# Kernel tuning notes

Hardware: AMD Instinct MI355X
Metric: run time of the kernel (lower is better)

The kernel has to match this reference:

```python
import jax, jax.numpy as jnp
import numpy as np

POS_IOU, NEG_IOU = 0.5, 0.4
VAR = (0.1, 0.1, 0.2, 0.2)
ALPHA = 1.0
B, A, C, G = 16, 65536, 81, 32


def setup_inputs() -> dict:
    key = jax.random.key(0)
    k1, k2, k3, k4, k5, k6, k7 = jax.random.split(key, 7)
    cls_logits = jax.random.normal(k1, (B, A, C), dtype=jnp.float32)
    bbox_regs = jax.random.normal(k2, (B, A, 4), dtype=jnp.float32)
    # anchors: normalized cx,cy in (0,1), w,h positive
    anc_cxy = jax.random.uniform(k3, (A, 2), minval=0.05, maxval=0.95)
    anc_wh = jax.random.uniform(k4, (A, 2), minval=0.02, maxval=0.30)
    anchors_cxcywh = jnp.concatenate([anc_cxy, anc_wh], axis=-1).astype(jnp.float32)
    # GT boxes: valid normalized xyxy built from random cxcywh
    g_cxy = jax.random.uniform(k5, (B, G, 2), minval=0.1, maxval=0.9)
    g_wh = jax.random.uniform(k6, (B, G, 2), minval=0.05, maxval=0.40)
    x1y1 = jnp.clip(g_cxy - g_wh / 2, 0.0, 1.0)
    x2y2 = jnp.clip(g_cxy + g_wh / 2, 0.0, 1.0)
    gt_boxes = jnp.concatenate([x1y1, x2y2], axis=-1).astype(jnp.float32)
    gt_labels = jax.random.randint(k7, (B, G), 1, C).astype(jnp.int64)
    gt_valid = jnp.ones((B, G), dtype=bool)
    return {"cls_logits": cls_logits, "bbox_regs": bbox_regs,
            "anchors_cxcywh": anchors_cxcywh, "gt_boxes": gt_boxes,
            "gt_labels": gt_labels, "gt_valid": gt_valid}


def _encode(gt_xyxy, anc_cxcywh):
    # gt_xyxy [B,A,4], anc_cxcywh [A,4] -> offsets [B,A,4]
    x1, y1, x2, y2 = jnp.split(gt_xyxy, 4, axis=-1)
    gx, gy = (x1 + x2) / 2, (y1 + y2) / 2
    gw = jnp.clip(x2 - x1, 1e-6, None)
    gh = jnp.clip(y2 - y1, 1e-6, None)
    ax, ay, aw, ah = (anc_cxcywh[None, :, i:i + 1] for i in range(4))
    dx = (gx - ax) / (aw * VAR[0])
    dy = (gy - ay) / (ah * VAR[1])
    dw = jnp.log(gw / aw) / VAR[2]
    dh = jnp.log(gh / ah) / VAR[3]
    return jnp.concatenate([dx, dy, dw, dh], axis=-1)


def _forward(cls_logits, bbox_regs, anchors_cxcywh, gt_boxes, gt_labels, gt_valid):
    ax, ay, aw, ah = (anchors_cxcywh[:, i] for i in range(4))
    anc_xyxy = jnp.stack([ax - aw / 2, ay - ah / 2, ax + aw / 2, ay + ah / 2], axis=-1)  # [A,4]
    # IoU [B,A,G] (assignment is torch.no_grad in the original)
    tl = jnp.maximum(anc_xyxy[None, :, None, :2], gt_boxes[:, None, :, :2])
    br = jnp.minimum(anc_xyxy[None, :, None, 2:], gt_boxes[:, None, :, 2:])
    wh = jnp.clip(br - tl, 0.0, None)
    inter = wh[..., 0] * wh[..., 1]
    area_a = jnp.clip(anc_xyxy[:, 2] - anc_xyxy[:, 0], 0.0, None) * jnp.clip(anc_xyxy[:, 3] - anc_xyxy[:, 1], 0.0, None)
    area_b = jnp.clip(gt_boxes[..., 2] - gt_boxes[..., 0], 0.0, None) * jnp.clip(gt_boxes[..., 3] - gt_boxes[..., 1], 0.0, None)
    iou = inter / (area_a[None, :, None] + area_b[:, None, :] - inter + 1e-9)
    iou = jnp.where(gt_valid[:, None, :], iou, -1.0)  # padded GTs never match
    iou = jax.lax.stop_gradient(iou)

    iou_max = jnp.max(iou, axis=-1)              # [B,A]
    iou_idx = jnp.argmax(iou, axis=-1)           # [B,A]
    pos = iou_max >= POS_IOU
    ign = (iou_max > NEG_IOU) & ~pos

    matched_boxes = jnp.take_along_axis(gt_boxes, iou_idx[..., None], axis=1)   # [B,A,4]
    matched_labels = jnp.take_along_axis(gt_labels, iou_idx, axis=1)            # [B,A]
    cls_t = jnp.where(pos, matched_labels, jnp.where(ign, -1, 0))               # [B,A]
    reg_t = jax.lax.stop_gradient(_encode(matched_boxes, anchors_cxcywh))       # [B,A,4]

    # classification CE over valid (non-ignored) anchors, per-image mean
    logp = jax.nn.log_softmax(cls_logits, axis=-1)
    tgt = jnp.clip(cls_t, 0, None)
    ce = -jnp.take_along_axis(logp, tgt[..., None], axis=-1)[..., 0]            # [B,A]
    valid = cls_t >= 0
    n_valid = jnp.sum(valid, axis=1)
    cls_per = jnp.sum(ce * valid, axis=1) / jnp.maximum(n_valid, 1)
    total_cls = jnp.sum(jnp.where(n_valid > 0, cls_per, 0.0))

    # smooth L1 over positive anchors, per-image mean over pos*4 elements
    d = jnp.abs(bbox_regs - reg_t)
    sl1 = jnp.where(d < 1.0, 0.5 * d * d, d - 0.5)                              # [B,A,4]
    n_pos = jnp.sum(pos, axis=1)
    reg_per = jnp.sum(sl1 * pos[..., None], axis=(1, 2)) / jnp.maximum(4 * n_pos, 1)
    total_reg = jnp.sum(jnp.where(n_pos > 0, reg_per, 0.0))

    return total_cls + ALPHA * total_reg


def reference(cls_logits, bbox_regs, anchors_cxcywh, gt_boxes, gt_labels, gt_valid):
    return _forward(cls_logits, bbox_regs, anchors_cxcywh, gt_boxes, gt_labels, gt_valid)
```

## Files before the change

kernel.cpp:

```cpp
#include <hip/hip_runtime.h>
#include <math.h>

constexpr int kB = 16;
constexpr int kA = 65536;
constexpr int kC = 81;
constexpr int kG = 32;
constexpr int kBlockA = 256;
constexpr float kPosIou = 0.5f;
constexpr float kNegIou = 0.4f;

__global__ __launch_bounds__(256) void ssd_main_kernel(
    const float* __restrict__ cls_logits,
    const float* __restrict__ bbox_regs,
    const float* __restrict__ anchors,
    const float* __restrict__ gt_boxes,
    const int*   __restrict__ gt_labels,
    const int*   __restrict__ gt_valid,
    float* __restrict__ ws)
{
    __shared__ float s_gx1[kG], s_gy1[kG], s_gx2[kG], s_gy2[kG], s_area[kG];
    __shared__ int   s_lab[kG], s_val[kG];
    __shared__ int   s_t[kBlockA];
    __shared__ float s_red[4][4];

    const int tid = threadIdx.x;
    const int blocks_per_b = kA / kBlockA;
    const int b  = blockIdx.x / blocks_per_b;
    const int a0 = (blockIdx.x % blocks_per_b) * kBlockA;

    if (tid < kG) {
        float4 gb = *reinterpret_cast<const float4*>(gt_boxes + ((size_t)b * kG + tid) * 4);
        s_gx1[tid] = gb.x; s_gy1[tid] = gb.y; s_gx2[tid] = gb.z; s_gy2[tid] = gb.w;
        s_area[tid] = fmaxf(gb.z - gb.x, 0.f) * fmaxf(gb.w - gb.y, 0.f);
        s_lab[tid] = gt_labels[b * kG + tid];
        s_val[tid] = gt_valid[b * kG + tid];
    }
    __syncthreads();

    const int a = a0 + tid;
    float4 anc = *reinterpret_cast<const float4*>(anchors + (size_t)a * 4);
    const float ax1 = anc.x - anc.z * 0.5f, ay1 = anc.y - anc.w * 0.5f;
    const float ax2 = anc.x + anc.z * 0.5f, ay2 = anc.y + anc.w * 0.5f;
    const float area_a = fmaxf(ax2 - ax1, 0.f) * fmaxf(ay2 - ay1, 0.f);

    float best = -2.0f;
    int   bidx = 0;
    #pragma unroll 8
    for (int g = 0; g < kG; ++g) {
        float tlx = fmaxf(ax1, s_gx1[g]);
        float tly = fmaxf(ay1, s_gy1[g]);
        float brx = fminf(ax2, s_gx2[g]);
        float bry = fminf(ay2, s_gy2[g]);
        float w = fmaxf(brx - tlx, 0.f);
        float h = fmaxf(bry - tly, 0.f);
        float inter = w * h;
        float iou = inter / (area_a + s_area[g] - inter + 1e-9f);
        iou = s_val[g] ? iou : -1.0f;
        if (iou > best) { best = iou; bidx = g; }
    }
    const bool pos = best >= kPosIou;
    const bool ign = (best > kNegIou) && !pos;
    const int cls_t = pos ? s_lab[bidx] : (ign ? -1 : 0);
    s_t[tid] = cls_t;

    float reg_sum = 0.f;
    if (pos) {
        float gx1 = s_gx1[bidx], gy1 = s_gy1[bidx], gx2 = s_gx2[bidx], gy2 = s_gy2[bidx];
        float gx = (gx1 + gx2) * 0.5f, gy = (gy1 + gy2) * 0.5f;
        float gw = fmaxf(gx2 - gx1, 1e-6f), gh = fmaxf(gy2 - gy1, 1e-6f);
        float dx = (gx - anc.x) / (anc.z * 0.1f);
        float dy = (gy - anc.y) / (anc.w * 0.1f);
        float dw = __logf(gw / anc.z) / 0.2f;
        float dh = __logf(gh / anc.w) / 0.2f;
        float4 br = *reinterpret_cast<const float4*>(bbox_regs + ((size_t)b * kA + a) * 4);
        float d0 = fabsf(br.x - dx), d1 = fabsf(br.y - dy);
        float d2 = fabsf(br.z - dw), d3 = fabsf(br.w - dh);
        reg_sum = (d0 < 1.f ? 0.5f * d0 * d0 : d0 - 0.5f)
                + (d1 < 1.f ? 0.5f * d1 * d1 : d1 - 0.5f)
                + (d2 < 1.f ? 0.5f * d2 * d2 : d2 - 0.5f)
                + (d3 < 1.f ? 0.5f * d3 * d3 : d3 - 0.5f);
    }
    __syncthreads();

    const int wave = tid >> 6;
    const int lane = tid & 63;
    const int g4   = lane >> 2;
    const int q    = lane & 3;
    float ce_acc = 0.f;

    #pragma unroll 2
    for (int it = 0; it < kBlockA / 64; ++it) {
        const int idx = it * 64 + wave * 16 + g4;
        const int ct  = s_t[idx];
        const float* row = cls_logits + ((size_t)b * kA + a0 + idx) * kC;

        float s = 0.f;
        #pragma unroll
        for (int k = 0; k < 5; ++k) {
            float4 v;
            __builtin_memcpy(&v, row + (k << 4) + (q << 2), 16);
            s += __expf(v.x) + __expf(v.y) + __expf(v.z) + __expf(v.w);
        }
        float tv = 0.f;
        if (q == 0) {
            s += __expf(row[80]);
            tv = row[ct < 0 ? 0 : ct];
        }
        s += __shfl_xor(s, 1);
        s += __shfl_xor(s, 2);
        if (q == 0 && ct >= 0)
            ce_acc += __logf(s) - tv;
    }

    float v0 = ce_acc;
    float v1 = (cls_t >= 0) ? 1.f : 0.f;
    float v2 = reg_sum;
    float v3 = pos ? 1.f : 0.f;
    #pragma unroll
    for (int off = 32; off > 0; off >>= 1) {
        v0 += __shfl_xor(v0, off);
        v1 += __shfl_xor(v1, off);
        v2 += __shfl_xor(v2, off);
        v3 += __shfl_xor(v3, off);
    }
    if (lane == 0) {
        s_red[wave][0] = v0; s_red[wave][1] = v1;
        s_red[wave][2] = v2; s_red[wave][3] = v3;
    }
    __syncthreads();
    if (tid < 4) {
        float acc = s_red[0][tid] + s_red[1][tid] + s_red[2][tid] + s_red[3][tid];
        atomicAdd(&ws[b * 4 + tid], acc);
    }
}

__global__ void ssd_final_kernel(const float* __restrict__ ws, float* __restrict__ out)
{
    const int lane = threadIdx.x;
    float v = 0.f;
    if (lane < kB) {
        float sce  = ws[lane * 4 + 0];
        float nval = ws[lane * 4 + 1];
        float ssl  = ws[lane * 4 + 2];
        float npos = ws[lane * 4 + 3];
        float cls = (nval > 0.f) ? sce / fmaxf(nval, 1.f) : 0.f;
        float reg = (npos > 0.f) ? ssl / fmaxf(4.f * npos, 1.f) : 0.f;
        v = cls + reg;
    }
    #pragma unroll
    for (int off = 1; off < kB; off <<= 1)
        v += __shfl_xor(v, off);
    if (lane == 0) out[0] = v;
}

extern "C" void kernel_launch(void* const* d_in, const int* in_sizes, int n_in,
                              void* d_out, int out_size, void* d_ws, size_t ws_size,
                              hipStream_t stream) {
    const float* cls_logits = (const float*)d_in[0];
    const float* bbox_regs  = (const float*)d_in[1];
    const float* anchors    = (const float*)d_in[2];
    const float* gt_boxes   = (const float*)d_in[3];
    const int*   gt_labels  = (const int*)d_in[4];
    const int*   gt_valid   = (const int*)d_in[5];
    float* ws  = (float*)d_ws;
    float* out = (float*)d_out;

    hipMemsetAsync(d_ws, 0, kB * 4 * sizeof(float), stream);

    ssd_main_kernel<<<dim3(kB * (kA / kBlockA)), dim3(kBlockA), 0, stream>>>(
        cls_logits, bbox_regs, anchors, gt_boxes, gt_labels, gt_valid, ws);
    ssd_final_kernel<<<dim3(1), dim3(64), 0, stream>>>(ws, out);
}
```

Before: 84.69 us.

## Stream logits with block-contiguous float4 loads and LDS atomic row sums

Each block now reads its contiguous 256x81 logits tile with fully coalesced float4 loads indexed linearly, computes exp per element and adds the results into per-row shared-memory sums. It uses LDS atomics spread over four banks in place of per-row 4-lane groups with misaligned loads. The per-batch global atomics and memset are replaced by per-block partial writes, which the final kernel reduces. The tradeoff is more LDS atomic traffic and an integer divide per float4 in exchange for better global memory coalescing.

New measurement: 144.5 us. +70.6%, slower.

```diff
diff --git a/kernel.cpp b/kernel.cpp
--- a/kernel.cpp
+++ b/kernel.cpp
@@ -6,8 +6,28 @@
 constexpr int kC = 81;
 constexpr int kG = 32;
 constexpr int kBlockA = 256;
+constexpr int kBlocksPerB = kA / kBlockA;
+constexpr int kSumStride = 264;
 constexpr float kPosIou = 0.5f;
 constexpr float kNegIou = 0.4f;
+
+__device__ __forceinline__ void accum_f4(float (*s_sum)[kSumStride], int bank,
+                                         const float* __restrict__ base, int j) {
+    float4 v = *reinterpret_cast<const float4*>(base + 4 * j);
+    const int f0 = 4 * j;
+    const int r = f0 / 81;
+    const int rem = f0 - r * 81;
+    const float e0 = __expf(v.x), e1 = __expf(v.y);
+    const float e2 = __expf(v.z), e3 = __expf(v.w);
+    if (rem <= 77) {
+        atomicAdd(&s_sum[bank][r], e0 + e1 + e2 + e3);
+    } else {
+        atomicAdd(&s_sum[bank][(f0 + 0) / 81], e0);
+        atomicAdd(&s_sum[bank][(f0 + 1) / 81], e1);
+        atomicAdd(&s_sum[bank][(f0 + 2) / 81], e2);
+        atomicAdd(&s_sum[bank][(f0 + 3) / 81], e3);
+    }
+}
 
 __global__ __launch_bounds__(256) void ssd_main_kernel(
     const float* __restrict__ cls_logits,
@@ -20,13 +40,12 @@
 {
     __shared__ float s_gx1[kG], s_gy1[kG], s_gx2[kG], s_gy2[kG], s_area[kG];
     __shared__ int   s_lab[kG], s_val[kG];
-    __shared__ int   s_t[kBlockA];
+    __shared__ float s_sum[4][kSumStride];
     __shared__ float s_red[4][4];
 
     const int tid = threadIdx.x;
-    const int blocks_per_b = kA / kBlockA;
-    const int b  = blockIdx.x / blocks_per_b;
-    const int a0 = (blockIdx.x % blocks_per_b) * kBlockA;
+    const int b  = blockIdx.x / kBlocksPerB;
+    const int a0 = (blockIdx.x % kBlocksPerB) * kBlockA;
 
     if (tid < kG) {
         float4 gb = *reinterpret_cast<const float4*>(gt_boxes + ((size_t)b * kG + tid) * 4);
@@ -34,6 +53,10 @@
         s_area[tid] = fmaxf(gb.z - gb.x, 0.f) * fmaxf(gb.w - gb.y, 0.f);
         s_lab[tid] = gt_labels[b * kG + tid];
         s_val[tid] = gt_valid[b * kG + tid];
+    }
+    {
+        float* p = &s_sum[0][0];
+        for (int i = tid; i < 4 * kSumStride; i += kBlockA) p[i] = 0.f;
     }
     __syncthreads();
 
@@ -61,7 +84,6 @@
     const bool pos = best >= kPosIou;
     const bool ign = (best > kNegIou) && !pos;
     const int cls_t = pos ? s_lab[bidx] : (ign ? -1 : 0);
-    s_t[tid] = cls_t;
 
     float reg_sum = 0.f;
     if (pos) {
@@ -80,39 +102,24 @@
                 + (d2 < 1.f ? 0.5f * d2 * d2 : d2 - 0.5f)
                 + (d3 < 1.f ? 0.5f * d3 * d3 : d3 - 0.5f);
     }
+
+    const float* base = cls_logits + ((size_t)b * kA + a0) * kC;
+    const float tv = base[(size_t)tid * kC + (cls_t < 0 ? 0 : cls_t)];
+
+    const int bank = tid & 3;
+    #pragma unroll 5
+    for (int k = 0; k < 20; ++k)
+        accum_f4(s_sum, bank, base, tid + (k << 8));
+    if (tid < 64)
+        accum_f4(s_sum, bank, base, 5120 + tid);
     __syncthreads();
+
+    const float S = s_sum[0][tid] + s_sum[1][tid] + s_sum[2][tid] + s_sum[3][tid];
+    const float ce = (cls_t >= 0) ? (__logf(S) - tv) : 0.f;
 
     const int wave = tid >> 6;
     const int lane = tid & 63;
-    const int g4   = lane >> 2;
-    const int q    = lane & 3;
-    float ce_acc = 0.f;
-
-    #pragma unroll 2
-    for (int it = 0; it < kBlockA / 64; ++it) {
-        const int idx = it * 64 + wave * 16 + g4;
-        const int ct  = s_t[idx];
-        const float* row = cls_logits + ((size_t)b * kA + a0 + idx) * kC;
-
-        float s = 0.f;
-        #pragma unroll
-        for (int k = 0; k < 5; ++k) {
-            float4 v;
-            __builtin_memcpy(&v, row + (k << 4) + (q << 2), 16);
-            s += __expf(v.x) + __expf(v.y) + __expf(v.z) + __expf(v.w);
-        }
-        float tv = 0.f;
-        if (q == 0) {
-            s += __expf(row[80]);
-            tv = row[ct < 0 ? 0 : ct];
-        }
-        s += __shfl_xor(s, 1);
-        s += __shfl_xor(s, 2);
-        if (q == 0 && ct >= 0)
-            ce_acc += __logf(s) - tv;
-    }
-
-    float v0 = ce_acc;
+    float v0 = ce;
     float v1 = (cls_t >= 0) ? 1.f : 0.f;
     float v2 = reg_sum;
     float v3 = pos ? 1.f : 0.f;
@@ -130,27 +137,43 @@
     __syncthreads();
     if (tid < 4) {
         float acc = s_red[0][tid] + s_red[1][tid] + s_red[2][tid] + s_red[3][tid];
-        atomicAdd(&ws[b * 4 + tid], acc);
+        ws[(size_t)blockIdx.x * 4 + tid] = acc;
     }
 }
 
-__global__ void ssd_final_kernel(const float* __restrict__ ws, float* __restrict__ out)
+__global__ __launch_bounds__(256) void ssd_final_kernel(
+    const float* __restrict__ ws, float* __restrict__ out)
 {
-    const int lane = threadIdx.x;
-    float v = 0.f;
-    if (lane < kB) {
-        float sce  = ws[lane * 4 + 0];
-        float nval = ws[lane * 4 + 1];
-        float ssl  = ws[lane * 4 + 2];
-        float npos = ws[lane * 4 + 3];
-        float cls = (nval > 0.f) ? sce / fmaxf(nval, 1.f) : 0.f;
-        float reg = (npos > 0.f) ? ssl / fmaxf(4.f * npos, 1.f) : 0.f;
-        v = cls + reg;
+    __shared__ float s_per_b[kB];
+    const int tid = threadIdx.x;
+    const int b = tid >> 4;
+    const int i = tid & 15;
+    float a0 = 0.f, a1 = 0.f, a2 = 0.f, a3 = 0.f;
+    #pragma unroll
+    for (int k = 0; k < 16; ++k) {
+        const float4 v = *reinterpret_cast<const float4*>(
+            ws + ((size_t)((b << 8) + (k << 4) + i)) * 4);
+        a0 += v.x; a1 += v.y; a2 += v.z; a3 += v.w;
     }
     #pragma unroll
-    for (int off = 1; off < kB; off <<= 1)
-        v += __shfl_xor(v, off);
-    if (lane == 0) out[0] = v;
+    for (int off = 1; off < 16; off <<= 1) {
+        a0 += __shfl_xor(a0, off);
+        a1 += __shfl_xor(a1, off);
+        a2 += __shfl_xor(a2, off);
+        a3 += __shfl_xor(a3, off);
+    }
+    if (i == 0) {
+        float cls = (a1 > 0.f) ? a0 / fmaxf(a1, 1.f) : 0.f;
+        float reg = (a3 > 0.f) ? a2 / fmaxf(4.f * a3, 1.f) : 0.f;
+        s_per_b[b] = cls + reg;
+    }
+    __syncthreads();
+    if (tid == 0) {
+        float t = 0.f;
+        #pragma unroll
+        for (int x = 0; x < kB; ++x) t += s_per_b[x];
+        out[0] = t;
+    }
 }
 
 extern "C" void kernel_launch(void* const* d_in, const int* in_sizes, int n_in,
@@ -165,9 +188,7 @@
     float* ws  = (float*)d_ws;
     float* out = (float*)d_out;
 
-    hipMemsetAsync(d_ws, 0, kB * 4 * sizeof(float), stream);
-
-    ssd_main_kernel<<<dim3(kB * (kA / kBlockA)), dim3(kBlockA), 0, stream>>>(
+    ssd_main_kernel<<<dim3(kB * kBlocksPerB), dim3(kBlockA), 0, stream>>>(
         cls_logits, bbox_regs, anchors, gt_boxes, gt_labels, gt_valid, ws);
-    ssd_final_kernel<<<dim3(1), dim3(64), 0, stream>>>(ws, out);
+    ssd_final_kernel<<<dim3(1), dim3(kBlockA), 0, stream>>>(ws, out);
 }
```
